# Kernel optimization log

Measured on AMD Instinct MI355X. Metric: run time of the kernel, lower is better.

The kernel has to match this reference:

```python
import jax, jax.numpy as jnp
import numpy as np

FEAT_STRIDE = 16
PRE_NMS = 6000   # TEST config
POST_NMS = 300
NMS_TH = 0.7


def _generate_anchors_3d(base_size=16, ratios=(0.5, 1.0, 2.0), scales=(8, 16, 32), time_dims=(16,)):
    """Standard Faster-RCNN anchor enumeration, extended with a time extent.
    Returns (A, 6) float32 boxes in [x1, y1, z1, x2, y2, z2] order (matches shift order)."""
    w = h = float(base_size)
    xc = yc = 0.5 * (base_size - 1)
    size = w * h
    ratios = np.asarray(ratios, dtype=np.float64)
    ws = np.round(np.sqrt(size / ratios))
    hs = np.round(ws * ratios)
    a2 = []
    for wi, hi in zip(ws, hs):
        for s in scales:
            ww, hh = wi * s, hi * s
            a2.append([xc - 0.5 * (ww - 1), yc - 0.5 * (hh - 1),
                       xc + 0.5 * (ww - 1), yc + 0.5 * (hh - 1)])
    out = []
    for t in time_dims:
        for a in a2:
            out.append([a[0], a[1], 0.0, a[2], a[3], float(t) - 1.0])
    return np.asarray(out, dtype=np.float32)


def setup_inputs() -> dict:
    key = jax.random.key(0)
    k1, k2 = jax.random.split(key)
    B, A, H, W, T = 2, 9, 32, 32, 16
    scores_map = jax.random.normal(k1, (B, 2 * A, H, W, T), dtype=jnp.float32)
    bbox_frame = jax.random.normal(k2, (B, 6 * A, H, W, T), dtype=jnp.float32) * 0.2
    im_info = jnp.array([512.0, 512.0, 16.0], dtype=jnp.float32)  # [img_h, img_w, n_frames]
    anchors = jnp.asarray(_generate_anchors_3d())  # (9, 6)
    return {"scores_map": scores_map, "bbox_frame": bbox_frame, "im_info": im_info, "anchors": anchors}


def _nms_single(boxes, scs):
    """Greedy 3D (spatio-temporal volume) NMS for one image.
    boxes: (N, 6), scs: (N,). Returns (POST_NMS, 7) rows [score, x1,y1,z1,x2,y2,z2],
    zero-padded past the number of kept proposals (matches output[i].zero_() + fill)."""
    order = jnp.argsort(-scs)[:PRE_NMS]           # descending score, pre-NMS top-k
    b = boxes[order]                              # (P, 6)
    s = scs[order]                                # (P,)
    vol = (b[:, 3] - b[:, 0] + 1.0) * (b[:, 4] - b[:, 1] + 1.0) * (b[:, 5] - b[:, 2] + 1.0)
    iw = jnp.clip(jnp.minimum(b[:, None, 3], b[None, :, 3]) - jnp.maximum(b[:, None, 0], b[None, :, 0]) + 1.0, 0.0)
    ih = jnp.clip(jnp.minimum(b[:, None, 4], b[None, :, 4]) - jnp.maximum(b[:, None, 1], b[None, :, 1]) + 1.0, 0.0)
    il = jnp.clip(jnp.minimum(b[:, None, 5], b[None, :, 5]) - jnp.maximum(b[:, None, 2], b[None, :, 2]) + 1.0, 0.0)
    inter = iw * ih * il                          # (P, P)
    iou = inter / (vol[:, None] + vol[None, :] - inter)
    iou = jax.lax.stop_gradient(iou)              # keep mask is non-differentiable
    P = b.shape[0]
    idx = jnp.arange(P)

    def step(keep, i):
        sup = (iou[i] > NMS_TH) & keep[i] & (idx > i)
        return keep & ~sup, None

    keep, _ = jax.lax.scan(step, jnp.ones((P,), dtype=bool), jnp.arange(P))
    rank = jnp.cumsum(keep) - 1
    pos = jnp.where(keep & (rank < POST_NMS), rank, POST_NMS)  # overflow slot POST_NMS
    rows = jnp.concatenate([s[:, None], b], axis=1)            # (P, 7)
    out = jnp.zeros((POST_NMS + 1, 7), dtype=boxes.dtype).at[pos].set(rows)
    return out[:POST_NMS]


def reference(scores_map, bbox_frame, im_info, anchors):
    A = anchors.shape[0]
    B = scores_map.shape[0]
    scores = scores_map[:, A:]                    # (B, A, H, W, T) foreground scores
    H, W, T = scores.shape[2], scores.shape[3], scores.shape[4]

    # --- anchor grid (matches np.meshgrid 'xy' + ravel = H-major, W, T order) ---
    sx = (jnp.arange(W) * FEAT_STRIDE).astype(scores_map.dtype)
    sy = (jnp.arange(H) * FEAT_STRIDE).astype(scores_map.dtype)
    sz = jnp.arange(T).astype(scores_map.dtype)
    X, Y, Z = jnp.meshgrid(sx, sy, sz)            # each (H, W, T)
    shift = jnp.stack([X.ravel(), Y.ravel(), Z.ravel()], axis=1)   # (K, 3)
    shifts = jnp.concatenate([shift, shift], axis=1)               # (K, 6)
    all_anchors = (anchors[None] + shifts[:, None]).reshape(-1, 6)  # (K*A, 6)

    deltas = bbox_frame.transpose(0, 2, 3, 4, 1).reshape(B, -1, 6)  # (B, K*A, 6)
    scs = scores.transpose(0, 2, 3, 4, 1).reshape(B, -1)            # (B, K*A)

    # --- bbox_transform_inv_3d ---
    aw = all_anchors[:, 3] - all_anchors[:, 0] + 1.0
    ah = all_anchors[:, 4] - all_anchors[:, 1] + 1.0
    al = all_anchors[:, 5] - all_anchors[:, 2] + 1.0
    acx = all_anchors[:, 0] + 0.5 * aw
    acy = all_anchors[:, 1] + 0.5 * ah
    acz = all_anchors[:, 2] + 0.5 * al
    pcx = deltas[..., 0] * aw + acx
    pcy = deltas[..., 1] * ah + acy
    pcz = deltas[..., 2] * al + acz
    pw = jnp.exp(deltas[..., 3]) * aw
    ph = jnp.exp(deltas[..., 4]) * ah
    pl = jnp.exp(deltas[..., 5]) * al
    proposals = jnp.stack([pcx - 0.5 * pw, pcy - 0.5 * ph, pcz - 0.5 * pl,
                           pcx + 0.5 * pw, pcy + 0.5 * ph, pcz + 0.5 * pl], axis=-1)

    # --- clip_boxes_3d: x in [0, img_w-1], y in [0, img_h-1], z in [0, n_frames-1] ---
    lim = jnp.stack([im_info[1], im_info[0], im_info[2],
                     im_info[1], im_info[0], im_info[2]]) - 1.0
    proposals = jnp.clip(proposals, 0.0, lim)

    return jax.vmap(_nms_single)(proposals, scs)  # (B, POST_NMS, 7)
```

## Files before the change

### kernel.cpp

```cpp
#include <hip/hip_runtime.h>
#include <stdint.h>

#define FEAT_STRIDE 16
#define PRE_NMS 6000
#define POST_NMS 300
#define NMS_TH 0.7f

static constexpr int B_ = 2, A_ = 9, H_ = 32, W_ = 32, T_ = 16;
static constexpr int LOC = H_ * W_ * T_;
static constexpr int N_ = LOC * A_;
static constexpr int NBIN = 65536;
static constexpr int NREP = 8;
static constexpr int CAP = 8192;
static constexpr int NW = 94;
static constexpr int ROWS = 6016;

static constexpr double BMID = 0.7000000178813934326171875;


__device__ __forceinline__ uint32_t f2u(float f) {
    uint32_t b = __float_as_uint(f);
    return b ^ ((b >> 31) ? 0xFFFFFFFFu : 0x80000000u);
}
__device__ __forceinline__ float u2f(uint32_t u) {
    uint32_t b = (u >> 31) ? (u ^ 0x80000000u) : ~u;
    return __uint_as_float(b);
}
__device__ __forceinline__ unsigned long long rl64(unsigned long long v, int lane) {
    unsigned int lo = (unsigned int)__builtin_amdgcn_readlane((int)(unsigned int)v, lane);
    unsigned int hi = (unsigned int)__builtin_amdgcn_readlane((int)(unsigned int)(v >> 32), lane);
    return ((unsigned long long)hi << 32) | lo;
}

__global__ void hist_kernel(const float* __restrict__ scores_map,
                            unsigned int* __restrict__ histR) {
    int gid = blockIdx.x * blockDim.x + threadIdx.x;
    if (gid >= B_ * N_) return;
    int b = gid / N_;
    int r = gid - b * N_;
    int a = r / LOC;
    int loc = r - a * LOC;
    float sc = scores_map[((size_t)(b * 2 * A_ + A_ + a)) * LOC + loc];
    uint32_t u = f2u(sc);
    int rep = blockIdx.x & (NREP - 1);
    atomicAdd(&histR[((size_t)(rep * B_ + b)) * NBIN + (u >> 16)], 1u);
}

__global__ void __launch_bounds__(256) partial_kernel(
        const unsigned int* __restrict__ histR,
        unsigned int* __restrict__ partials) {
    int c = blockIdx.x, bb = blockIdx.y, t = threadIdx.x;
    unsigned int s = 0;
#pragma unroll
    for (int r = 0; r < NREP; ++r) {
        const uint4* h4 = reinterpret_cast<const uint4*>(
            histR + ((size_t)(r * B_ + bb)) * NBIN + c * 1024);
        uint4 v = h4[t];
        s += v.x + v.y + v.z + v.w;
    }
    __shared__ unsigned int red[256];
    red[t] = s;
    __syncthreads();
    for (int off = 128; off > 0; off >>= 1) {
        if (t < off) red[t] += red[t + off];
        __syncthreads();
    }
    if (t == 0) partials[bb * 64 + c] = red[0];
}

__global__ void __launch_bounds__(256) rewrite_kernel(
        const unsigned int* __restrict__ histR,
        unsigned int* __restrict__ hist,
        unsigned int* __restrict__ binbase,
        const unsigned int* __restrict__ partials,
        unsigned int* __restrict__ thr) {
    int c = blockIdx.x, bb = blockIdx.y, t = threadIdx.x;
    __shared__ unsigned int sp[64];
    __shared__ unsigned int ssum[256];
    if (t < 64) sp[t] = partials[bb * 64 + t];
    uint4 v = {0u, 0u, 0u, 0u};
#pragma unroll
    for (int r = 0; r < NREP; ++r) {
        const uint4* h4 = reinterpret_cast<const uint4*>(
            histR + ((size_t)(r * B_ + bb)) * NBIN + c * 1024);
        uint4 w = h4[t];
        v.x += w.x; v.y += w.y; v.z += w.z; v.w += w.w;
    }
    unsigned int* h = hist + (size_t)bb * NBIN + c * 1024;
    unsigned int* bs = binbase + (size_t)bb * NBIN + c * 1024;
    ssum[t] = v.x + v.y + v.z + v.w;
    __syncthreads();
    unsigned int chunkBase = 0;
    for (int q = c + 1; q < 64; ++q) chunkBase += sp[q];
    for (int off = 1; off < 256; off <<= 1) {
        unsigned int val = (t + off < 256) ? ssum[t + off] : 0u;
        __syncthreads();
        ssum[t] += val;
        __syncthreads();
    }
    unsigned int run = chunkBase + ((t < 255) ? ssum[t + 1] : 0u);
    unsigned int cnt[4] = {v.x, v.y, v.z, v.w};
    unsigned int offv[4];
    for (int q = 3; q >= 0; --q) {
        offv[q] = run;
        unsigned int newrun = run + cnt[q];
        if (run < (unsigned)PRE_NMS && newrun >= (unsigned)PRE_NMS) {
            thr[bb * 2 + 0] = (unsigned)(c * 1024 + t * 4 + q);
            thr[bb * 2 + 1] = newrun;
        }
        run = newrun;
    }
    uint4 o4 = {offv[0], offv[1], offv[2], offv[3]};
    reinterpret_cast<uint4*>(h)[t] = o4;
    reinterpret_cast<uint4*>(bs)[t] = o4;
}

__global__ void __launch_bounds__(256) compact_kernel(
        const float* __restrict__ scores_map,
        const unsigned int* __restrict__ thr,
        unsigned long long* __restrict__ cand,
        unsigned int* __restrict__ hist) {
    int tid = threadIdx.x;
    int gid = blockIdx.x * 256 + tid;
    int b = gid / N_;
    int r = gid - b * N_;
    int a = r / LOC;
    int loc = r - a * LOC;
    float sc = scores_map[((size_t)(b * 2 * A_ + A_ + a)) * LOC + loc];
    uint32_t u = f2u(sc);
    uint32_t bin = u >> 16;
    if (bin >= thr[b * 2]) {
        int n = loc * A_ + a;
        unsigned long long key = ((unsigned long long)u << 18)
                               | (unsigned long long)(N_ - 1 - n);
        unsigned int slot = atomicAdd(&hist[b * NBIN + bin], 1u);
        if (slot < (unsigned)CAP)
            cand[(size_t)b * CAP + slot] = key;
    }
}

__global__ void __launch_bounds__(256) bucket_decode(
        const unsigned long long* __restrict__ cand,
        const unsigned int* __restrict__ hist,
        const unsigned int* __restrict__ binbase,
        const unsigned int* __restrict__ thr,
        const float* __restrict__ bbox_frame,
        const float* __restrict__ im_info,
        const float* __restrict__ anchors,
        float* __restrict__ sortedBox) {
    int gid = blockIdx.x * 256 + threadIdx.x;
    int bb = gid / CAP;
    int i = gid - bb * CAP;
    int count = (int)thr[bb * 2 + 1];
    if (count > CAP) count = CAP;
    if (i >= count) return;
    const unsigned long long* cb = cand + (size_t)bb * CAP;
    unsigned long long me = cb[i];
    int bin = (int)(me >> 34);
    int start = (int)binbase[bb * NBIN + bin];
    int end = (int)hist[bb * NBIN + bin];
    if (end > count) end = count;
    int rank = start;
    for (int q = start; q < end; ++q)
        rank += (cb[q] > me);
    if (rank >= PRE_NMS) return;

    uint32_t u = (uint32_t)(me >> 18);
    int n = N_ - 1 - (int)(me & 0x3FFFFull);
    int a = n % A_;
    int loc = n / A_;
    int k = loc % T_;
    int j = (loc / T_) % W_;
    int ii = loc / (T_ * W_);

    float ax1 = anchors[a * 6 + 0] + (float)(FEAT_STRIDE * j);
    float ay1 = anchors[a * 6 + 1] + (float)(FEAT_STRIDE * ii);
    float az1 = anchors[a * 6 + 2] + (float)k;
    float ax2 = anchors[a * 6 + 3] + (float)(FEAT_STRIDE * j);
    float ay2 = anchors[a * 6 + 4] + (float)(FEAT_STRIDE * ii);
    float az2 = anchors[a * 6 + 5] + (float)k;
    float aw = ax2 - ax1 + 1.0f, ah = ay2 - ay1 + 1.0f, al = az2 - az1 + 1.0f;
    float acx = ax1 + 0.5f * aw, acy = ay1 + 0.5f * ah, acz = az1 + 0.5f * al;

    const float* dp = bbox_frame + ((size_t)(bb * 6 * A_ + a * 6)) * LOC
                    + ii * (W_ * T_) + j * T_ + k;
    float d0 = dp[0 * LOC], d1 = dp[1 * LOC], d2 = dp[2 * LOC];
    float d3 = dp[3 * LOC], d4 = dp[4 * LOC], d5 = dp[5 * LOC];

    float pcx = d0 * aw + acx, pcy = d1 * ah + acy, pcz = d2 * al + acz;
    float pw = expf(d3) * aw, ph = expf(d4) * ah, pl = expf(d5) * al;

    float x1 = pcx - 0.5f * pw, y1 = pcy - 0.5f * ph, z1 = pcz - 0.5f * pl;
    float x2 = pcx + 0.5f * pw, y2 = pcy + 0.5f * ph, z2 = pcz + 0.5f * pl;

    float lx = im_info[1] - 1.0f, ly = im_info[0] - 1.0f, lz = im_info[2] - 1.0f;
    x1 = fminf(fmaxf(x1, 0.0f), lx); y1 = fminf(fmaxf(y1, 0.0f), ly); z1 = fminf(fmaxf(z1, 0.0f), lz);
    x2 = fminf(fmaxf(x2, 0.0f), lx); y2 = fminf(fmaxf(y2, 0.0f), ly); z2 = fminf(fmaxf(z2, 0.0f), lz);

    float vol = (x2 - x1 + 1.0f) * (y2 - y1 + 1.0f) * (z2 - z1 + 1.0f);
    float* p = sortedBox + ((size_t)bb * ROWS + rank) * 8;
    p[0] = x1; p[1] = y1; p[2] = z1; p[3] = x2;
    p[4] = y2; p[5] = z2; p[6] = vol; p[7] = u2f(u);
}

__global__ void mask_build(const float* __restrict__ sortedBox,
                           unsigned long long* __restrict__ mask,
                           unsigned long long* __restrict__ band) {
    int g = blockIdx.x / NW, w = blockIdx.x % NW;
    if (w < g) return;
    int bb = blockIdx.y;
    int lane = threadIdx.x;
    __shared__ float4 colA[64];
    __shared__ float4 colB[64];
    const float* sb = sortedBox + (size_t)bb * ROWS * 8;
    int col = w * 64 + lane;
    if (col < PRE_NMS) {
        const float4* cp4 = reinterpret_cast<const float4*>(sb + (size_t)col * 8);
        float4 lo = cp4[0], hi = cp4[1];
        colA[lane] = make_float4(lo.x, lo.y, lo.z, lo.w);
        colB[lane] = make_float4(hi.x, hi.y, hi.z, 0.0f);
    } else {
        colA[lane] = make_float4(3e8f, 0.0f, 0.0f, -3e8f);
        colB[lane] = make_float4(0.0f, 0.0f, 1.0f, 0.0f);
    }
    __syncthreads();
    int row = g * 64 + lane;
    if (row >= PRE_NMS) return;
    const float4* rp4 = reinterpret_cast<const float4*>(sb + (size_t)row * 8);
    float4 rlo = rp4[0], rhi = rp4[1];
    float x1 = rlo.x, y1 = rlo.y, z1 = rlo.z;
    float x2 = rlo.w, y2 = rhi.x, z2 = rhi.y, v = rhi.z;
    unsigned long long word = 0;
#pragma unroll 8
    for (int b2 = 0; b2 < 64; ++b2) {
        float4 cA = colA[b2];
        float4 cB = colB[b2];
        float iw = fminf(x2, cA.w) - fmaxf(x1, cA.x) + 1.0f;
        float ih = fminf(y2, cB.x) - fmaxf(y1, cA.y) + 1.0f;
        float il = fminf(z2, cB.y) - fmaxf(z1, cA.z) + 1.0f;
        iw = fmaxf(iw, 0.0f); ih = fmaxf(ih, 0.0f); il = fmaxf(il, 0.0f);
        float inter = iw * ih * il;
        float denom = v + cB.z - inter;
        bool over = ((double)inter >= BMID * (double)denom);
        int cidx = w * 64 + b2;
        if (cidx > row && over) word |= (1ull << b2);
    }
    mask[((size_t)bb * NW + w) * ROWS + row] = word;
    unsigned long long* bd = band + ((size_t)bb * ROWS + row) * 4;
    if (w == g) {
        bd[0] = word;
        if (g + 1 >= NW) bd[1] = 0ull;
        if (g + 2 >= NW) bd[2] = 0ull;
        if (g + 3 >= NW) bd[3] = 0ull;
    }
    if (w == g + 1) bd[1] = word;
    if (w == g + 2) bd[2] = word;
    if (w == g + 3) bd[3] = word;
}

__global__ void __launch_bounds__(256) suppress_kernel(
        const unsigned long long* __restrict__ mask,
        const unsigned long long* __restrict__ band,
        const float* __restrict__ sortedBox,
        float* __restrict__ out) {
    int bb = blockIdx.x;
    int tid = threadIdx.x;
    int lane = tid & 63, wv = tid >> 6;
    __shared__ int keptAll[POST_NMS];
    __shared__ int stotal;

    const unsigned long long* M  = mask + (size_t)bb * NW * ROWS;
    const unsigned long long* Bd = band + (size_t)bb * ROWS * 4;
    const float* sb = sortedBox + (size_t)bb * ROWS * 8;
    float* ob = out + (size_t)bb * POST_NMS * 7;

    if (wv == 0) {
        const unsigned long long* rowp0 = M + (size_t)lane * ROWS;
        int l1 = lane + 64; if (l1 > NW - 1) l1 = NW - 1;
        const unsigned long long* rowp1 = M + (size_t)l1 * ROWS;

        unsigned long long r0 = 0, r1 = 0;
        if (lane == NW - 1 - 64)
            r1 = ~((1ull << (PRE_NMS - (NW - 1) * 64)) - 1ull);

        unsigned long long pend[4][8][2];
#pragma unroll
        for (int q = 0; q < 4; ++q)
#pragma unroll
            for (int i = 0; i < 8; ++i) { pend[q][i][0] = 0; pend[q][i][1] = 0; }

        unsigned long long bd0[3], bd1[3], bd2[3], bd3[3];
#define BAND_LOAD(CH, BD)                                                      \
        {   const ulonglong2* bp_ = reinterpret_cast<const ulonglong2*>(       \
                &Bd[(size_t)((CH) * 64 + lane) * 4]);                          \
            ulonglong2 va_ = bp_[0];                                           \
            BD[0] = va_.x; BD[1] = va_.y;                                      \
            BD[2] = Bd[(size_t)((CH) * 64 + lane) * 4 + 2]; }
        BAND_LOAD(0, bd0)
        BAND_LOAD(1, bd1)
        BAND_LOAD(2, bd2)
        BAND_LOAD(3, bd3)

        unsigned long long supCur = 0, S1 = 0, S2 = 0;
        int kt = 0;
        bool stop = false;

#define CHUNK_BODY(CVAL, P, BD)                                                \
        if (!stop) {                                                          \
            const int c = (CVAL);                                             \
            {             \
                unsigned long long a0 = 0, a1 = 0;                            \
                _Pragma("unroll")                                              \
                for (int i = 0; i < 8; ++i) {                                  \
                    a0 |= pend[((P) + 1) & 3][i][0];                           \
                    a1 |= pend[((P) + 1) & 3][i][1];                           \
                }                                                              \
                r0 |= a0; r1 |= a1;                                            \
                _Pragma("unroll")                                              \
                for (int i = 0; i < 8; ++i) {                                  \
                    pend[((P) + 1) & 3][i][0] = 0;                             \
                    pend[((P) + 1) & 3][i][1] = 0;                             \
                }                                                              \
            }                                                                  \
            unsigned long long cur = (c < 64) ? rl64(r0, c) : rl64(r1, c - 64);\
            unsigned long long alive = ~(cur | supCur);                        \
            int nk = 0;                                                        \
            _Pragma("unroll")                                                  \
            for (int i = 0; i < 8; ++i) {                                      \
                if (alive && kt + nk < POST_NMS) {                             \
                    int b_ = (int)__builtin_ctzll(alive);                      \
                    int bs = __builtin_amdgcn_readfirstlane(b_);               \
                    int R = c * 64 + bs;                                       \
                    if (lane == 0) keptAll[kt + nk] = R;                       \
                    unsigned long long dr = rl64(BD[0], bs);                   \
                    S1 |= rl64(BD[1], bs);                                     \
                    S2 |= rl64(BD[2], bs);                                     \
                    pend[(P)][i][0] = rowp0[R];                                \
                    pend[(P)][i][1] = rowp1[R];                                \
                    ++nk;                                                      \
                    alive &= ~(dr | (1ull << bs));                             \
                }                                                              \
            }                                                                  \
            kt += nk;                                                          \
            while (alive && kt < POST_NMS) {         \
                unsigned long long o00 = 0, o01 = 0, o10 = 0, o11 = 0,         \
                                   o20 = 0, o21 = 0, o30 = 0, o31 = 0;         \
                _Pragma("unroll")                                              \
                for (int i = 0; i < 4; ++i) {                                  \
                    if (alive && kt < POST_NMS) {                              \
                        int b_ = (int)__builtin_ctzll(alive);                  \
                        int bs = __builtin_amdgcn_readfirstlane(b_);           \
                        int R = c * 64 + bs;                                   \
                        if (lane == 0) keptAll[kt] = R;                        \
                        unsigned long long dr = rl64(BD[0], bs);               \
                        S1 |= rl64(BD[1], bs);                                 \
                        S2 |= rl64(BD[2], bs);                                 \
                        if (i == 0)      { o00 = rowp0[R]; o01 = rowp1[R]; }   \
                        else if (i == 1) { o10 = rowp0[R]; o11 = rowp1[R]; }   \
                        else if (i == 2) { o20 = rowp0[R]; o21 = rowp1[R]; }   \
                        else             { o30 = rowp0[R]; o31 = rowp1[R]; }   \
                        ++kt;                                                  \
                        alive &= ~(dr | (1ull << bs));                         \
                    }                                                          \
                }                                                              \
                r0 |= o00 | o10 | o20 | o30;                                   \
                r1 |= o01 | o11 | o21 | o31;                                   \
            }                                                                  \
            if (kt >= POST_NMS) stop = true;                                   \
            supCur = S1; S1 = S2; S2 = 0;                                      \
            if (c + 4 < NW) BAND_LOAD(c + 4, BD)                               \
        }

        for (int cb = 0; cb < 92; cb += 4) {
            CHUNK_BODY(cb + 0, 0, bd0)
            CHUNK_BODY(cb + 1, 1, bd1)
            CHUNK_BODY(cb + 2, 2, bd2)
            CHUNK_BODY(cb + 3, 3, bd3)
        }
        CHUNK_BODY(92, 0, bd0)
        CHUNK_BODY(93, 1, bd1)
#undef CHUNK_BODY
#undef BAND_LOAD
        if (lane == 0) stotal = kt;
    }
    __syncthreads();

    int total = stotal;
    for (int e = tid; e < total * 7; e += 256) {
        int i = e / 7, j = e - i * 7;
        ob[e] = sb[(size_t)keptAll[i] * 8 + (j == 0 ? 7 : j - 1)];
    }
    for (int idx = total * 7 + tid; idx < POST_NMS * 7; idx += 256)
        ob[idx] = 0.0f;
}

extern "C" void kernel_launch(void* const* d_in, const int* in_sizes, int n_in,
                              void* d_out, int out_size, void* d_ws, size_t ws_size,
                              hipStream_t stream) {
    const float* scores_map = (const float*)d_in[0];
    const float* bbox_frame = (const float*)d_in[1];
    const float* im_info    = (const float*)d_in[2];
    const float* anchors    = (const float*)d_in[3];
    float* out = (float*)d_out;

    char* ws = (char*)d_ws;
    unsigned long long* mask  = (unsigned long long*)(ws + 0);
    unsigned int* binbase     = (unsigned int*)(ws + 0);
    unsigned int* histR       = (unsigned int*)(ws + 524288);
    float* sortedBox          = (float*)(ws + 9048064);
    unsigned long long* cand  = (unsigned long long*)(ws + 9433088);
    unsigned int* hist        = (unsigned int*)(ws + 9564160);
    unsigned long long* band  = (unsigned long long*)(ws + 9564160);
    unsigned int* thr         = (unsigned int*)(ws + 10088448);
    unsigned int* partials    = (unsigned int*)(ws + 10088464);

    hipMemsetAsync(histR, 0, (size_t)NREP * B_ * NBIN * 4, stream);

    int total = B_ * N_;
    hist_kernel<<<(total + 255) / 256, 256, 0, stream>>>(scores_map, histR);
    partial_kernel<<<dim3(64, B_), 256, 0, stream>>>(histR, partials);
    rewrite_kernel<<<dim3(64, B_), 256, 0, stream>>>(histR, hist, binbase, partials, thr);
    compact_kernel<<<total / 256, 256, 0, stream>>>(scores_map, thr, cand, hist);
    bucket_decode<<<B_ * CAP / 256, 256, 0, stream>>>(cand, hist, binbase, thr,
                                                      bbox_frame, im_info, anchors,
                                                      sortedBox);
    mask_build<<<dim3(NW * NW, B_), 64, 0, stream>>>(sortedBox, mask, band);
    suppress_kernel<<<B_, 256, 0, stream>>>(mask, band, sortedBox, out);
}
```

Before: 136.4 us.

## Restructure NMS suppress pipeline with blocked mask layout and deferred row loads

New measurement: 160.1 us. +17.4%, slower.

```diff
diff --git a/kernel.cpp b/kernel.cpp
--- a/kernel.cpp
+++ b/kernel.cpp
@@ -48,18 +48,20 @@
 
 __global__ void __launch_bounds__(256) partial_kernel(
         const unsigned int* __restrict__ histR,
+        unsigned int* __restrict__ hist,
         unsigned int* __restrict__ partials) {
     int c = blockIdx.x, bb = blockIdx.y, t = threadIdx.x;
-    unsigned int s = 0;
+    uint4 acc = {0u, 0u, 0u, 0u};
 #pragma unroll
     for (int r = 0; r < NREP; ++r) {
         const uint4* h4 = reinterpret_cast<const uint4*>(
             histR + ((size_t)(r * B_ + bb)) * NBIN + c * 1024);
         uint4 v = h4[t];
-        s += v.x + v.y + v.z + v.w;
-    }
+        acc.x += v.x; acc.y += v.y; acc.z += v.z; acc.w += v.w;
+    }
+    reinterpret_cast<uint4*>(hist + (size_t)bb * NBIN + c * 1024)[t] = acc;
     __shared__ unsigned int red[256];
-    red[t] = s;
+    red[t] = acc.x + acc.y + acc.z + acc.w;
     __syncthreads();
     for (int off = 128; off > 0; off >>= 1) {
         if (t < off) red[t] += red[t + off];
@@ -69,7 +71,6 @@
 }
 
 __global__ void __launch_bounds__(256) rewrite_kernel(
-        const unsigned int* __restrict__ histR,
         unsigned int* __restrict__ hist,
         unsigned int* __restrict__ binbase,
         const unsigned int* __restrict__ partials,
@@ -78,16 +79,9 @@
     __shared__ unsigned int sp[64];
     __shared__ unsigned int ssum[256];
     if (t < 64) sp[t] = partials[bb * 64 + t];
-    uint4 v = {0u, 0u, 0u, 0u};
-#pragma unroll
-    for (int r = 0; r < NREP; ++r) {
-        const uint4* h4 = reinterpret_cast<const uint4*>(
-            histR + ((size_t)(r * B_ + bb)) * NBIN + c * 1024);
-        uint4 w = h4[t];
-        v.x += w.x; v.y += w.y; v.z += w.z; v.w += w.w;
-    }
     unsigned int* h = hist + (size_t)bb * NBIN + c * 1024;
     unsigned int* bs = binbase + (size_t)bb * NBIN + c * 1024;
+    uint4 v = reinterpret_cast<const uint4*>(h)[t];
     ssum[t] = v.x + v.y + v.z + v.w;
     __syncthreads();
     unsigned int chunkBase = 0;
@@ -245,7 +239,7 @@
         int cidx = w * 64 + b2;
         if (cidx > row && over) word |= (1ull << b2);
     }
-    mask[((size_t)bb * NW + w) * ROWS + row] = word;
+    mask[(((size_t)bb * NW + g) * NW + w) * 64 + lane] = word;
     unsigned long long* bd = band + ((size_t)bb * ROWS + row) * 4;
     if (w == g) {
         bd[0] = word;
@@ -258,139 +252,125 @@
     if (w == g + 3) bd[3] = word;
 }
 
-__global__ void __launch_bounds__(256) suppress_kernel(
+__global__ void __launch_bounds__(64) suppress_kernel(
         const unsigned long long* __restrict__ mask,
         const unsigned long long* __restrict__ band,
         const float* __restrict__ sortedBox,
         float* __restrict__ out) {
     int bb = blockIdx.x;
-    int tid = threadIdx.x;
-    int lane = tid & 63, wv = tid >> 6;
+    int lane = threadIdx.x;
     __shared__ int keptAll[POST_NMS];
-    __shared__ int stotal;
-
-    const unsigned long long* M  = mask + (size_t)bb * NW * ROWS;
+
+    const unsigned long long* M  = mask + (size_t)bb * NW * NW * 64;
     const unsigned long long* Bd = band + (size_t)bb * ROWS * 4;
     const float* sb = sortedBox + (size_t)bb * ROWS * 8;
     float* ob = out + (size_t)bb * POST_NMS * 7;
 
-    if (wv == 0) {
-        const unsigned long long* rowp0 = M + (size_t)lane * ROWS;
-        int l1 = lane + 64; if (l1 > NW - 1) l1 = NW - 1;
-        const unsigned long long* rowp1 = M + (size_t)l1 * ROWS;
-
-        unsigned long long r0 = 0, r1 = 0;
-        if (lane == NW - 1 - 64)
-            r1 = ~((1ull << (PRE_NMS - (NW - 1) * 64)) - 1ull);
-
-        unsigned long long pend[4][8][2];
+    int w1c = lane + 64; if (w1c > NW - 1) w1c = NW - 1;
+
+    unsigned long long r0 = 0, r1 = 0;
+    if (lane == NW - 1 - 64)
+        r1 = ~((1ull << (PRE_NMS - (NW - 1) * 64)) - 1ull);
+
+    unsigned long long pend[4][4][2];
 #pragma unroll
-        for (int q = 0; q < 4; ++q)
+    for (int q = 0; q < 4; ++q)
 #pragma unroll
-            for (int i = 0; i < 8; ++i) { pend[q][i][0] = 0; pend[q][i][1] = 0; }
-
-        unsigned long long bd0[3], bd1[3], bd2[3], bd3[3];
+        for (int s = 0; s < 4; ++s) { pend[q][s][0] = 0; pend[q][s][1] = 0; }
+
+    unsigned long long bd0[4], bd1[4], bd2[4], bd3[4];
 #define BAND_LOAD(CH, BD)                                                      \
-        {   const ulonglong2* bp_ = reinterpret_cast<const ulonglong2*>(       \
-                &Bd[(size_t)((CH) * 64 + lane) * 4]);                          \
-            ulonglong2 va_ = bp_[0];                                           \
-            BD[0] = va_.x; BD[1] = va_.y;                                      \
-            BD[2] = Bd[(size_t)((CH) * 64 + lane) * 4 + 2]; }
-        BAND_LOAD(0, bd0)
-        BAND_LOAD(1, bd1)
-        BAND_LOAD(2, bd2)
-        BAND_LOAD(3, bd3)
-
-        unsigned long long supCur = 0, S1 = 0, S2 = 0;
-        int kt = 0;
-        bool stop = false;
-
-#define CHUNK_BODY(CVAL, P, BD)                                                \
-        if (!stop) {                                                          \
-            const int c = (CVAL);                                             \
-            {             \
-                unsigned long long a0 = 0, a1 = 0;                            \
-                _Pragma("unroll")                                              \
-                for (int i = 0; i < 8; ++i) {                                  \
-                    a0 |= pend[((P) + 1) & 3][i][0];                           \
-                    a1 |= pend[((P) + 1) & 3][i][1];                           \
-                }                                                              \
-                r0 |= a0; r1 |= a1;                                            \
-                _Pragma("unroll")                                              \
-                for (int i = 0; i < 8; ++i) {                                  \
-                    pend[((P) + 1) & 3][i][0] = 0;                             \
-                    pend[((P) + 1) & 3][i][1] = 0;                             \
-                }                                                              \
+    {   const ulonglong2* bp_ = reinterpret_cast<const ulonglong2*>(           \
+            &Bd[(size_t)((CH) * 64 + lane) * 4]);                              \
+        ulonglong2 vA_ = bp_[0], vB_ = bp_[1];                                 \
+        BD[0] = vA_.x; BD[1] = vA_.y; BD[2] = vB_.x; BD[3] = vB_.y; }
+    BAND_LOAD(0, bd0)
+    BAND_LOAD(1, bd1)
+    BAND_LOAD(2, bd2)
+    BAND_LOAD(3, bd3)
+
+    unsigned long long supCur = 0, S1 = 0, S2 = 0, S3 = 0;
+    const unsigned long long* lastA = M;
+    int kt = 0;
+    bool stop = false;
+
+#define CHUNK_BODY(CVAL, PS, BD)                                               \
+    if (!stop) {                                                              \
+        const int c = (CVAL);                                                 \
+           \
+        r0 |= pend[PS][0][0] | pend[PS][1][0] | pend[PS][2][0] | pend[PS][3][0]; \
+        r1 |= pend[PS][0][1] | pend[PS][1][1] | pend[PS][2][1] | pend[PS][3][1]; \
+        unsigned long long cur = (c < 64) ? rl64(r0, c) : rl64(r1, c - 64);   \
+        unsigned long long alive = ~(cur | supCur);                           \
+        const unsigned long long* a0 = lastA;                                 \
+        const unsigned long long* a1 = lastA;                                 \
+        const unsigned long long* a2 = lastA;                                 \
+        const unsigned long long* a3 = lastA;                                 \
+        _Pragma("unroll")                                                      \
+        for (int s = 0; s < 4; ++s) {                                          \
+            if (alive && kt < POST_NMS) {                                      \
+                int b_ = (int)__builtin_ctzll(alive);                          \
+                int bs = __builtin_amdgcn_readfirstlane(b_);                   \
+                if (lane == 0) keptAll[kt] = c * 64 + bs;                      \
+                unsigned long long dr = rl64(BD[0], bs);                       \
+                S1 |= rl64(BD[1], bs);                                         \
+                S2 |= rl64(BD[2], bs);                                         \
+                S3 |= rl64(BD[3], bs);                                         \
+                const unsigned long long* rb =                                 \
+                    M + ((size_t)c * NW) * 64 + bs;                            \
+                if (s == 0) a0 = rb; else if (s == 1) a1 = rb;                 \
+                else if (s == 2) a2 = rb; else a3 = rb;                        \
+                lastA = rb;                                                    \
+                ++kt;                                                          \
+                alive &= ~(dr | (1ull << bs));                                 \
             }                                                                  \
-            unsigned long long cur = (c < 64) ? rl64(r0, c) : rl64(r1, c - 64);\
-            unsigned long long alive = ~(cur | supCur);                        \
-            int nk = 0;                                                        \
-            _Pragma("unroll")                                                  \
-            for (int i = 0; i < 8; ++i) {                                      \
-                if (alive && kt + nk < POST_NMS) {                             \
-                    int b_ = (int)__builtin_ctzll(alive);                      \
-                    int bs = __builtin_amdgcn_readfirstlane(b_);               \
-                    int R = c * 64 + bs;                                       \
-                    if (lane == 0) keptAll[kt + nk] = R;                       \
-                    unsigned long long dr = rl64(BD[0], bs);                   \
-                    S1 |= rl64(BD[1], bs);                                     \
-                    S2 |= rl64(BD[2], bs);                                     \
-                    pend[(P)][i][0] = rowp0[R];                                \
-                    pend[(P)][i][1] = rowp1[R];                                \
-                    ++nk;                                                      \
-                    alive &= ~(dr | (1ull << bs));                             \
-                }                                                              \
-            }                                                                  \
-            kt += nk;                                                          \
-            while (alive && kt < POST_NMS) {         \
-                unsigned long long o00 = 0, o01 = 0, o10 = 0, o11 = 0,         \
-                                   o20 = 0, o21 = 0, o30 = 0, o31 = 0;         \
-                _Pragma("unroll")                                              \
-                for (int i = 0; i < 4; ++i) {                                  \
-                    if (alive && kt < POST_NMS) {                              \
-                        int b_ = (int)__builtin_ctzll(alive);                  \
-                        int bs = __builtin_amdgcn_readfirstlane(b_);           \
-                        int R = c * 64 + bs;                                   \
-                        if (lane == 0) keptAll[kt] = R;                        \
-                        unsigned long long dr = rl64(BD[0], bs);               \
-                        S1 |= rl64(BD[1], bs);                                 \
-                        S2 |= rl64(BD[2], bs);                                 \
-                        if (i == 0)      { o00 = rowp0[R]; o01 = rowp1[R]; }   \
-                        else if (i == 1) { o10 = rowp0[R]; o11 = rowp1[R]; }   \
-                        else if (i == 2) { o20 = rowp0[R]; o21 = rowp1[R]; }   \
-                        else             { o30 = rowp0[R]; o31 = rowp1[R]; }   \
-                        ++kt;                                                  \
-                        alive &= ~(dr | (1ull << bs));                         \
-                    }                                                          \
-                }                                                              \
-                r0 |= o00 | o10 | o20 | o30;                                   \
-                r1 |= o01 | o11 | o21 | o31;                                   \
-            }                                                                  \
-            if (kt >= POST_NMS) stop = true;                                   \
-            supCur = S1; S1 = S2; S2 = 0;                                      \
-            if (c + 4 < NW) BAND_LOAD(c + 4, BD)                               \
-        }
-
-        for (int cb = 0; cb < 92; cb += 4) {
-            CHUNK_BODY(cb + 0, 0, bd0)
-            CHUNK_BODY(cb + 1, 1, bd1)
-            CHUNK_BODY(cb + 2, 2, bd2)
-            CHUNK_BODY(cb + 3, 3, bd3)
-        }
-        CHUNK_BODY(92, 0, bd0)
-        CHUNK_BODY(93, 1, bd1)
+        }                                                                      \
+        while (alive && kt < POST_NMS) {           \
+            int b_ = (int)__builtin_ctzll(alive);                              \
+            int bs = __builtin_amdgcn_readfirstlane(b_);                       \
+            if (lane == 0) keptAll[kt] = c * 64 + bs;                          \
+            unsigned long long dr = rl64(BD[0], bs);                           \
+            S1 |= rl64(BD[1], bs);                                             \
+            S2 |= rl64(BD[2], bs);                                             \
+            S3 |= rl64(BD[3], bs);                                             \
+            const unsigned long long* rb = M + ((size_t)c * NW) * 64 + bs;     \
+            r0 |= rb[(size_t)lane * 64];                                       \
+            r1 |= rb[(size_t)w1c * 64];                                        \
+            lastA = rb;                                                        \
+            ++kt;                                                              \
+            alive &= ~(dr | (1ull << bs));                                     \
+        }                                                                      \
+        if (kt >= POST_NMS) stop = true;                                       \
+        supCur = S1; S1 = S2; S2 = S3; S3 = 0;                                 \
+                      \
+        pend[PS][0][0] = a0[(size_t)lane * 64];                                \
+        pend[PS][0][1] = a0[(size_t)w1c * 64];                                 \
+        pend[PS][1][0] = a1[(size_t)lane * 64];                                \
+        pend[PS][1][1] = a1[(size_t)w1c * 64];                                 \
+        pend[PS][2][0] = a2[(size_t)lane * 64];                                \
+        pend[PS][2][1] = a2[(size_t)w1c * 64];                                 \
+        pend[PS][3][0] = a3[(size_t)lane * 64];                                \
+        pend[PS][3][1] = a3[(size_t)w1c * 64];                                 \
+                    \
+        if (c + 4 < NW) BAND_LOAD(c + 4, BD)                                   \
+    }
+
+    for (int cb = 0; cb < 92; cb += 4) {
+        CHUNK_BODY(cb + 0, 0, bd0)
+        CHUNK_BODY(cb + 1, 1, bd1)
+        CHUNK_BODY(cb + 2, 2, bd2)
+        CHUNK_BODY(cb + 3, 3, bd3)
+    }
+    CHUNK_BODY(92, 0, bd0)
+    CHUNK_BODY(93, 1, bd1)
 #undef CHUNK_BODY
 #undef BAND_LOAD
-        if (lane == 0) stotal = kt;
-    }
-    __syncthreads();
-
-    int total = stotal;
-    for (int e = tid; e < total * 7; e += 256) {
+
+    for (int e = lane; e < kt * 7; e += 64) {
         int i = e / 7, j = e - i * 7;
         ob[e] = sb[(size_t)keptAll[i] * 8 + (j == 0 ? 7 : j - 1)];
     }
-    for (int idx = total * 7 + tid; idx < POST_NMS * 7; idx += 256)
+    for (int idx = kt * 7 + lane; idx < POST_NMS * 7; idx += 64)
         ob[idx] = 0.0f;
 }
 
@@ -418,12 +398,12 @@
 
     int total = B_ * N_;
     hist_kernel<<<(total + 255) / 256, 256, 0, stream>>>(scores_map, histR);
-    partial_kernel<<<dim3(64, B_), 256, 0, stream>>>(histR, partials);
-    rewrite_kernel<<<dim3(64, B_), 256, 0, stream>>>(histR, hist, binbase, partials, thr);
+    partial_kernel<<<dim3(64, B_), 256, 0, stream>>>(histR, hist, partials);
+    rewrite_kernel<<<dim3(64, B_), 256, 0, stream>>>(hist, binbase, partials, thr);
     compact_kernel<<<total / 256, 256, 0, stream>>>(scores_map, thr, cand, hist);
     bucket_decode<<<B_ * CAP / 256, 256, 0, stream>>>(cand, hist, binbase, thr,
                                                       bbox_frame, im_info, anchors,
                                                       sortedBox);
     mask_build<<<dim3(NW * NW, B_), 64, 0, stream>>>(sortedBox, mask, band);
-    suppress_kernel<<<B_, 256, 0, stream>>>(mask, band, sortedBox, out);
-}
+    suppress_kernel<<<B_, 64, 0, stream>>>(mask, band, sortedBox, out);
+}
```
